# Kernel optimization log

Hardware: AMD Instinct MI355X
Metric: run time of the kernel (lower is better)

Reference implementation:

```python
import jax, jax.numpy as jnp
import numpy as np

N = 16384; C = 16; H = 256; W = 704
HEADS = 4; PTS = 4; K = 8; DH = C // HEADS
EPS = 1e-3  # BatchNorm eps from module

def _bn(x, g, b):
    # BatchNorm1d in training mode: batch statistics over N
    mu = x.mean(axis=0)
    var = x.var(axis=0)
    return (x - mu) * jax.lax.rsqrt(var + EPS) * g + b

def setup_inputs():
    key = jax.random.key(0)
    ks = jax.random.split(key, 20)
    def w(i, shape, s=0.25):
        return jax.random.normal(ks[i], shape, jnp.float32) * s
    grid_y = jax.random.randint(ks[0], (N,), 0, H)
    grid_x = jax.random.randint(ks[1], (N,), 0, W)
    return {
        "point_features": jax.random.normal(ks[2], (N, C), jnp.float32),
        "image_feat": jax.random.normal(ks[3], (C, H, W), jnp.float32),
        "image_grid": jnp.stack([grid_y, grid_x], axis=1),
        "Wk": w(4, (C, C)), "bk": w(5, (C,)), "gk": jnp.ones((C,)), "betak": jnp.zeros((C,)),
        "Wfc": w(6, (2, C)), "bfc": w(7, (C,)), "gfc": jnp.ones((C,)), "betafc": jnp.zeros((C,)),
        "Wt": w(8, (C, C)), "bt": w(9, (C,)), "gt": jnp.ones((C,)), "betat": jnp.zeros((C,)),
        "Woff": w(10, (C, HEADS * PTS * 2), 0.02), "boff": w(11, (HEADS * PTS * 2,), 0.5),
        "Wattn": w(12, (C, HEADS * PTS), 0.02), "battn": jnp.zeros((HEADS * PTS,)),
        "Wval": w(13, (C, C)), "bval": w(14, (C,)),
        "Wout": w(15, (C, C)), "bout": w(16, (C,)),
        "Wf": w(17, (2 * C, C)), "bf": w(18, (C,)), "gf": jnp.ones((C,)), "betaf": jnp.zeros((C,)),
    }

def _deform_attn(q, image_feat, grid_f, Woff, boff, Wattn, battn, Wval, bval, Wout, bout):
    # MSDeformAttn with 1 level: learned offsets around projected pixel, bilinear sampling
    n = q.shape[0]
    off = (q @ Woff + boff).reshape(n, HEADS, PTS, 2)
    attn = jax.nn.softmax((q @ Wattn + battn).reshape(n, HEADS, PTS), axis=-1)
    val = (image_feat.reshape(C, H * W).T @ Wval + bval).reshape(H * W, HEADS, DH)
    val_h = val.transpose(1, 0, 2)  # [HEADS, HW, DH]
    loc_y = grid_f[:, 0][:, None, None] + off[..., 0]  # [N, HEADS, PTS]
    loc_x = grid_f[:, 1][:, None, None] + off[..., 1]
    y0 = jnp.floor(loc_y); x0 = jnp.floor(loc_x)
    wy = loc_y - y0; wx = loc_x - x0

    def corner(yi, xi, wgt):
        valid = (yi >= 0) & (yi <= H - 1) & (xi >= 0) & (xi <= W - 1)
        yc = jnp.clip(yi, 0, H - 1).astype(jnp.int32)
        xc = jnp.clip(xi, 0, W - 1).astype(jnp.int32)
        idx = (yc * W + xc).transpose(1, 0, 2)  # [HEADS, N, PTS]
        g = jax.vmap(lambda v, i: v[i])(val_h, idx)  # [HEADS, N, PTS, DH]
        return g * (wgt * valid).transpose(1, 0, 2)[..., None]

    samp = (corner(y0, x0, (1 - wy) * (1 - wx))
            + corner(y0, x0 + 1, (1 - wy) * wx)
            + corner(y0 + 1, x0, wy * (1 - wx))
            + corner(y0 + 1, x0 + 1, wy * wx))  # [HEADS, N, PTS, DH]
    out = (samp * attn.transpose(1, 0, 2)[..., None]).sum(axis=2)  # [HEADS, N, DH]
    out = out.transpose(1, 0, 2).reshape(n, C)
    return out @ Wout + bout

def reference(point_features, image_feat, image_grid, Wk, bk, gk, betak, Wfc, bfc, gfc, betafc, Wt, bt, gt, betat, Woff, boff, Wattn, battn, Wval, bval, Wout, bout, Wf, bf, gf, betaf):
    grid_f = image_grid.astype(jnp.float32)
    # KNN over projected pixel coords (cKDTree.query k=K+1, drop self)
    d2 = ((grid_f[:, None, :] - grid_f[None, :, :]) ** 2).sum(-1)
    _, nidx = jax.lax.top_k(-d2, K + 1)
    nidx = nidx[:, 1:]  # [N, K]

    pts = _bn(point_features @ Wk + bk, gk, betak)  # pts_key_proj
    # normalized relative image-plane positions -> fc
    center = grid_f.mean(axis=0)
    rel = grid_f - center
    mx = jnp.abs(rel).max(axis=0)
    mx = jnp.where(mx == 0, 1.0, mx)
    pos = _bn((rel / mx) @ Wfc + bfc, gfc, betafc)

    # gather image feats at projected pixels + KNN-graph neighbor aggregation
    gathered = image_feat[:, image_grid[:, 0], image_grid[:, 1]].T  # [N, C]
    neigh = gathered[nidx].mean(axis=1)  # [N, C]

    q = pts + pos
    img_pre = _deform_attn(q, image_feat, grid_f, Woff, boff, Wattn, battn, Wval, bval, Wout, bout) + neigh

    pts_pre = _bn(pts @ Wt + bt, gt, betat)  # pts_transform
    fuse = jax.nn.relu(jnp.concatenate([pts_pre, img_pre], axis=-1))  # activate_out
    return jax.nn.relu(_bn(fuse @ Wf + bf, gf, betaf))  # fuse_conv
```

## Files before the change

kernel.cpp:

```cpp
#include <hip/hip_runtime.h>
#include <climits>

#define N_ 16384
#define C_ 16
#define H_ 256
#define W_ 704
#define HW_ (H_*W_)
#define NC_ (N_*C_)
#define EPS_ 1e-3f
#define HDR_ 512

typedef unsigned long long ull;


#define VAL_  (HDR_ + 9*NC_)
#define KNNI_ (VAL_ + HW_*16)
#define PARTF_ (KNNI_ + 378256)

__device__ __forceinline__ float wsum64(float v){
#pragma unroll
  for (int o = 32; o > 0; o >>= 1) v += __shfl_down(v, o);
  return v;
}

#define LOAD16(dst, src) { const float4* _s=(const float4*)(src); float4 _a=_s[0],_b=_s[1],_c=_s[2],_d=_s[3]; \
  dst[0]=_a.x;dst[1]=_a.y;dst[2]=_a.z;dst[3]=_a.w; dst[4]=_b.x;dst[5]=_b.y;dst[6]=_b.z;dst[7]=_b.w; \
  dst[8]=_c.x;dst[9]=_c.y;dst[10]=_c.z;dst[11]=_c.w; dst[12]=_d.x;dst[13]=_d.y;dst[14]=_d.z;dst[15]=_d.w; }

#define STORE16(dst, src) { float4* _d=(float4*)(dst); \
  _d[0]=make_float4(src[0],src[1],src[2],src[3]); _d[1]=make_float4(src[4],src[5],src[6],src[7]); \
  _d[2]=make_float4(src[8],src[9],src[10],src[11]); _d[3]=make_float4(src[12],src[13],src[14],src[15]); }

__global__ __launch_bounds__(256) void k_init(float* ws){
  if (blockIdx.x < 176){
    int4* c = (int4*)(ws + KNNI_);
    c[blockIdx.x*256 + threadIdx.x] = make_int4(0,0,0,0);
  } else if (threadIdx.x == 0){
    int* ih = (int*)ws;
    ih[0]=0; ih[1]=0; ih[2]=INT_MAX; ih[3]=INT_MIN; ih[4]=INT_MAX; ih[5]=INT_MIN;
  }
}

__global__ __launch_bounds__(256) void k_gridcnt(const int* __restrict__ grid, float* __restrict__ ws){
  int i = blockIdx.x*256 + threadIdx.x;
  int2 p = ((const int2*)grid)[i];
  int* counts = (int*)(ws + KNNI_);
  atomicAdd(&counts[p.x*W_ + p.y], 1);
  int sy=p.x, sx=p.y, mny=p.x, mxy=p.x, mnx=p.y, mxx=p.y;
#pragma unroll
  for (int o=32;o>0;o>>=1){
    sy += __shfl_down(sy,o); sx += __shfl_down(sx,o);
    mny = min(mny,__shfl_down(mny,o)); mxy = max(mxy,__shfl_down(mxy,o));
    mnx = min(mnx,__shfl_down(mnx,o)); mxx = max(mxx,__shfl_down(mxx,o));
  }
  __shared__ int sh[24];
  int w = threadIdx.x >> 6;
  if ((threadIdx.x & 63) == 0){
    sh[w]=sy; sh[4+w]=sx; sh[8+w]=mny; sh[12+w]=mxy; sh[16+w]=mnx; sh[20+w]=mxx;
  }
  __syncthreads();
  if (threadIdx.x == 0){
    int a0=sh[0]+sh[1]+sh[2]+sh[3];
    int a1=sh[4]+sh[5]+sh[6]+sh[7];
    int a2=min(min(sh[8],sh[9]),min(sh[10],sh[11]));
    int a3=max(max(sh[12],sh[13]),max(sh[14],sh[15]));
    int a4=min(min(sh[16],sh[17]),min(sh[18],sh[19]));
    int a5=max(max(sh[20],sh[21]),max(sh[22],sh[23]));
    int* ih = (int*)ws;
    atomicAdd(&ih[0],a0); atomicAdd(&ih[1],a1);
    atomicMin(&ih[2],a2); atomicMax(&ih[3],a3);
    atomicMin(&ih[4],a4); atomicMax(&ih[5],a5);
  }
}

__global__ __launch_bounds__(256) void k_scanA(float* ws){
  const int* counts = (const int*)(ws + KNNI_);
  int* bsum = (int*)(ws + KNNI_) + 180224 + 180240;
  int t = threadIdx.x;
  int v = counts[blockIdx.x*256 + t];
#pragma unroll
  for (int o=32;o>0;o>>=1) v += __shfl_down(v,o);
  __shared__ int w4[4];
  if ((t&63)==0) w4[t>>6] = v;
  __syncthreads();
  if (t==0) bsum[blockIdx.x] = w4[0]+w4[1]+w4[2]+w4[3];
}

__global__ __launch_bounds__(256) void k_scanB(float* ws){
  if (threadIdx.x == 0){
    int* ih = (int*)ws;
    float cy = (float)ih[0] / (float)N_;
    float cx = (float)ih[1] / (float)N_;
    float my = fmaxf((float)ih[3]-cy, cy-(float)ih[2]);
    float mx = fmaxf((float)ih[5]-cx, cx-(float)ih[4]);
    if (my == 0.f) my = 1.f;
    if (mx == 0.f) mx = 1.f;
    ws[264]=cy; ws[265]=cx; ws[266]=1.f/my; ws[267]=1.f/mx;
  }
  int* bsum = (int*)(ws + KNNI_) + 180224 + 180240;
  int* boff = bsum + 704;
  __shared__ int tmp[256];
  __shared__ int carry;
  int t = threadIdx.x;
  if (t==0) carry = 0;
  __syncthreads();
  for (int c=0;c<3;++c){
    int idx = c*256 + t;
    int v = (idx < 704) ? bsum[idx] : 0;
    tmp[t] = v;
    __syncthreads();
    for (int o=1;o<256;o<<=1){
      int x = (t>=o) ? tmp[t-o] : 0;
      __syncthreads();
      tmp[t] += x;
      __syncthreads();
    }
    int incl = tmp[t];
    int base = carry;
    if (idx < 704) boff[idx] = base + incl - v;
    __syncthreads();
    if (t==255) carry = base + incl;
    __syncthreads();
  }
}

__global__ __launch_bounds__(256) void k_scanC(float* ws){
  int* counts = (int*)(ws + KNNI_);
  int* cellst = counts + 180224;
  const int* boff = counts + 180224 + 180240 + 704;
  __shared__ int tmp[256];
  int t = threadIdx.x;
  int i = blockIdx.x*256 + t;
  int v = counts[i];
  tmp[t] = v;
  __syncthreads();
  for (int o=1;o<256;o<<=1){
    int x = (t>=o) ? tmp[t-o] : 0;
    __syncthreads();
    tmp[t] += x;
    __syncthreads();
  }
  int start = boff[blockIdx.x] + tmp[t] - v;
  cellst[i] = start;
  counts[i] = start;
  if (i == 0) cellst[HW_] = N_;
}

__global__ __launch_bounds__(256) void k_scatter(const int* __restrict__ grid, float* __restrict__ ws){
  int i = blockIdx.x*256 + threadIdx.x;
  int2 g = ((const int2*)grid)[i];
  int* counts = (int*)(ws + KNNI_);
  unsigned* psort = (unsigned*)(counts + 180224 + 180240 + 704 + 704);
  int pos = atomicAdd(&counts[g.x*W_ + g.y], 1);
  psort[pos] = ((unsigned)g.x<<24) | ((unsigned)g.y<<14) | (unsigned)i;
}

__global__ __launch_bounds__(256) void k_gath(const float* __restrict__ imf,
                                              const int* __restrict__ grid,
                                              float* __restrict__ ws){
  int idx = blockIdx.x*256 + threadIdx.x;
  int i = idx >> 4, c = idx & 15;
  int2 g = ((const int2*)grid)[i];
  ws[HDR_ + 2*NC_ + idx] = imf[c*HW_ + g.x*W_ + g.y];
}

__global__ __launch_bounds__(64) void k_knn2(float* __restrict__ ws){
  int gid = blockIdx.x*64 + threadIdx.x;
  const int* cellst = (const int*)(ws + KNNI_) + 180224;
  const unsigned* psort = (const unsigned*)((const int*)(ws + KNNI_) + 180224 + 180240 + 704 + 704);
  unsigned me = psort[gid];
  int y = (int)(me>>24), x = (int)((me>>14)&1023), i = (int)(me&16383);
  int r = 8;
  for (;;){
    int y0=max(y-r,0), y1=min(y+r,H_-1), x0=max(x-r,0), x1=min(x+r,W_-1);
    bool covered = (y0==0)&&(y1==H_-1)&&(x0==0)&&(x1==W_-1);
    int area = (y1-y0+1)*(x1-x0+1);
    if (area >= 224 || covered) break;
    r += 8;
  }
  ull arr[9];
  for (;;){
    int y0=max(y-r,0), y1=min(y+r,H_-1), x0=max(x-r,0), x1=min(x+r,W_-1);
    bool covered = (y0==0)&&(y1==H_-1)&&(x0==0)&&(x1==W_-1);
#pragma unroll
    for (int q=0;q<9;++q) arr[q] = ~0ull;
    for (int yy=y0; yy<=y1; ++yy){
      int rowb = yy*W_;
      int s = cellst[rowb + x0];
      int e = cellst[rowb + x1 + 1];
      for (int p=s; p<e; ++p){
        unsigned u = psort[p];
        int py = (int)(u>>24), px = (int)((u>>14)&1023), pi = (int)(u&16383);
        int dy = y-py, dx = x-px;
        int d2 = dy*dy + dx*dx;
        ull key = ((ull)(unsigned)d2 << 14) | (unsigned)pi;
        if (key < arr[8]){
          int q = 8;
          while (q > 0 && arr[q-1] > key){ arr[q] = arr[q-1]; --q; }
          arr[q] = key;
        }
      }
    }
    if (covered) break;
    if (arr[8] != ~0ull){
      int d9 = (int)(arr[8] >> 14);
      if (d9 < (r+1)*(r+1)) break;
    }
    r <<= 1;
  }
  const float* gath = ws + HDR_ + 2*NC_;
  float acc[16];
#pragma unroll
  for (int c=0;c<16;++c) acc[c] = 0.f;
  for (int nb=1; nb<9; ++nb){
    int idx = (int)(arr[nb] & 16383ull);
    const float4* s4 = (const float4*)(gath + idx*16);
#pragma unroll
    for (int rq=0; rq<4; ++rq){
      float4 v = s4[rq];
      acc[rq*4]+=v.x; acc[rq*4+1]+=v.y; acc[rq*4+2]+=v.z; acc[rq*4+3]+=v.w;
    }
  }
  float* neigh = ws + HDR_ + 7*NC_;
  float o[16];
#pragma unroll
  for (int c=0;c<16;++c) o[c] = acc[c]*0.125f;
  STORE16(neigh + i*16, o);
}

__global__ __launch_bounds__(64) void k_lin1(
    const float* __restrict__ pf, const int* __restrict__ grid,
    const float* __restrict__ Wk, const float* __restrict__ bk,
    const float* __restrict__ Wfc, const float* __restrict__ bfc,
    float* __restrict__ ws)
{
  __shared__ float sWk[256], sbk[16], sWfc[32], sbfc[16];
  int t = threadIdx.x;
  for (int j=t;j<256;j+=64) sWk[j] = Wk[j];
  if (t < 16){ sbk[t]=bk[t]; sbfc[t]=bfc[t]; }
  if (t < 32) sWfc[t] = Wfc[t];
  __syncthreads();
  int i = blockIdx.x*64 + t;
  float p[16]; LOAD16(p, pf + i*16);
  float ok[16];
#pragma unroll
  for (int c=0;c<16;++c) ok[c] = sbk[c];
#pragma unroll
  for (int j=0;j<16;++j){ float v = p[j];
#pragma unroll
    for (int c=0;c<16;++c) ok[c] += v*sWk[j*16+c];
  }
  float* pts_lin = ws + HDR_;
  STORE16(pts_lin + i*16, ok);
  float cy=ws[264], cx=ws[265], imy=ws[266], imx=ws[267];
  int2 g = ((const int2*)grid)[i];
  float ry = ((float)g.x - cy)*imy, rx = ((float)g.y - cx)*imx;
  float op[16];
#pragma unroll
  for (int c=0;c<16;++c) op[c] = ry*sWfc[c] + rx*sWfc[16+c] + sbfc[c];
  float* pos_lin = ws + HDR_ + NC_;
  STORE16(pos_lin + i*16, op);
  float* partK  = ws + VAL_;
  float* partFC = ws + VAL_ + 8192;
#pragma unroll
  for (int c=0;c<16;++c){
    float a = wsum64(ok[c]); float b = wsum64(ok[c]*ok[c]);
    if (t==0){ partK[blockIdx.x*32+c]=a; partK[blockIdx.x*32+16+c]=b; }
    a = wsum64(op[c]); b = wsum64(op[c]*op[c]);
    if (t==0){ partFC[blockIdx.x*32+c]=a; partFC[blockIdx.x*32+16+c]=b; }
  }
}

__device__ __forceinline__ void red1_body(const float* __restrict__ g, const float* __restrict__ b,
                                          float* __restrict__ ws, int partOff, int aOff, float* red){
  int t = threadIdx.x, slot = t & 31, chunk = t >> 5;
  const float* part = ws + partOff;
  float acc = 0.f;
  for (int bb=chunk*32; bb<chunk*32+32; ++bb) acc += part[bb*32 + slot];
  red[t] = acc;
  __syncthreads();
  if (chunk == 0){
    float v = red[slot];
#pragma unroll
    for (int k2=1;k2<8;++k2) v += red[k2*32+slot];
    red[slot] = v;
  }
  __syncthreads();
  if (t < 16){
    float mu  = red[t]    * (1.f/N_);
    float var = red[16+t] * (1.f/N_) - mu*mu;
    float a = g[t] / sqrtf(var + EPS_);
    ws[aOff+t]    = a;
    ws[aOff+16+t] = b[t] - mu*a;
  }
  __syncthreads();
}

__global__ __launch_bounds__(256) void k_red2(const float* __restrict__ gk, const float* __restrict__ betak,
                                              const float* __restrict__ gfc, const float* __restrict__ betafc,
                                              float* __restrict__ ws){
  __shared__ float red[256];
  red1_body(gk, betak, ws, VAL_, 136, red);
  red1_body(gfc, betafc, ws, VAL_+8192, 168, red);
}

__global__ __launch_bounds__(256) void k_red1(const float* __restrict__ g, const float* __restrict__ b,
                                              float* __restrict__ ws, int partOff, int aOff){
  __shared__ float red[256];
  red1_body(g, b, ws, partOff, aOff, red);
}

__global__ __launch_bounds__(64) void k_qstage(
    const float* __restrict__ Wt, const float* __restrict__ bt,
    const float* __restrict__ Woff, const float* __restrict__ boff,
    const float* __restrict__ Wattn, const float* __restrict__ battn,
    float* __restrict__ ws)
{
  __shared__ float sWt[256], sWoff[512], sWattn[256];
  __shared__ float sbt[16], sboff[32], sbattn[16];
  __shared__ float skA[16], skC[16], sfcA[16], sfcC[16];
  int t = threadIdx.x;
  for (int j=t;j<256;j+=64){ sWt[j]=Wt[j]; sWattn[j]=Wattn[j]; }
  for (int j=t;j<512;j+=64) sWoff[j]=Woff[j];
  if (t<16){ sbt[t]=bt[t]; sbattn[t]=battn[t];
    skA[t]=ws[136+t]; skC[t]=ws[152+t]; sfcA[t]=ws[168+t]; sfcC[t]=ws[184+t]; }
  if (t<32) sboff[t]=boff[t];
  __syncthreads();
  int i = blockIdx.x*64 + t;
  float* pts_lin = ws + HDR_;
  float* pos_lin = ws + HDR_ + NC_;
  float* t_lin   = ws + HDR_ + 3*NC_;
  float* offp    = ws + HDR_ + 4*NC_;
  float* attnp   = ws + HDR_ + 6*NC_;
  float pl[16], po[16];
  LOAD16(pl, pts_lin + i*16);
  LOAD16(po, pos_lin + i*16);
  float pts[16], q[16];
#pragma unroll
  for (int c=0;c<16;++c){ pts[c] = pl[c]*skA[c]+skC[c]; q[c] = pts[c] + po[c]*sfcA[c]+sfcC[c]; }
  float tv[16];
#pragma unroll
  for (int c=0;c<16;++c) tv[c] = sbt[c];
#pragma unroll
  for (int j=0;j<16;++j){ float v=pts[j];
#pragma unroll
    for (int c=0;c<16;++c) tv[c] += v*sWt[j*16+c];
  }
  STORE16(t_lin + i*16, tv);
  float* partT = ws + VAL_ + 16384;
#pragma unroll
  for (int c=0;c<16;++c){
    float a = wsum64(tv[c]); float b = wsum64(tv[c]*tv[c]);
    if (t==0){ partT[blockIdx.x*32+c]=a; partT[blockIdx.x*32+16+c]=b; }
  }
  float ov[32];
#pragma unroll
  for (int o=0;o<32;++o) ov[o] = sboff[o];
#pragma unroll
  for (int j=0;j<16;++j){ float v=q[j];
#pragma unroll
    for (int o=0;o<32;++o) ov[o] += v*sWoff[j*32+o];
  }
  { float4* d=(float4*)(offp + i*32);
#pragma unroll
    for (int r=0;r<8;++r) d[r]=make_float4(ov[r*4],ov[r*4+1],ov[r*4+2],ov[r*4+3]);
  }
  float l[16];
#pragma unroll
  for (int c=0;c<16;++c) l[c] = sbattn[c];
#pragma unroll
  for (int j=0;j<16;++j){ float v=q[j];
#pragma unroll
    for (int c=0;c<16;++c) l[c] += v*sWattn[j*16+c];
  }
  float av[16];
#pragma unroll
  for (int h=0;h<4;++h){
    float m = fmaxf(fmaxf(l[h*4],l[h*4+1]),fmaxf(l[h*4+2],l[h*4+3]));
    float e0=expf(l[h*4]-m), e1=expf(l[h*4+1]-m), e2=expf(l[h*4+2]-m), e3=expf(l[h*4+3]-m);
    float inv = 1.f/(e0+e1+e2+e3);
    av[h*4]=e0*inv; av[h*4+1]=e1*inv; av[h*4+2]=e2*inv; av[h*4+3]=e3*inv;
  }
  STORE16(attnp + i*16, av);
}

__global__ __launch_bounds__(256) void k_val(const float* __restrict__ imf,
    const float* __restrict__ Wval, const float* __restrict__ bval, float* __restrict__ ws)
{
  __shared__ float sW[256], sb[16];
  int t = threadIdx.x;
  sW[t] = Wval[t];
  if (t < 16) sb[t] = bval[t];
  __syncthreads();
  int pix = blockIdx.x*256 + t;
  float a[16];
#pragma unroll
  for (int ci=0;ci<16;++ci) a[ci] = imf[ci*HW_ + pix];
  float o[16];
#pragma unroll
  for (int c=0;c<16;++c) o[c] = sb[c];
#pragma unroll
  for (int ci=0;ci<16;++ci){ float v=a[ci];
#pragma unroll
    for (int c=0;c<16;++c) o[c] += v*sW[ci*16+c];
  }
  float* val = ws + VAL_;
  STORE16(val + pix*16, o);
}

__global__ __launch_bounds__(256) void k_attn(
    const int* __restrict__ grid,
    const float* __restrict__ Wout, const float* __restrict__ bout,
    const float* __restrict__ Wf, const float* __restrict__ bf,
    float* __restrict__ ws)
{
  __shared__ float sWout[256], sWf[512], sbout[16], sbf[16];
  __shared__ float sTl[1024], sNei[1024], sSamp[1024], sImg[1024];
  __shared__ float sPart[128];
  int t = threadIdx.x;
  int p = t >> 2, h = t & 3;
  int i = blockIdx.x*64 + p;
  sWout[t]=Wout[t]; sWf[t]=Wf[t]; sWf[t+256]=Wf[t+256];
  if (t<16){ sbout[t]=bout[t]; sbf[t]=bf[t]; }
  {
    const float4* tl4 = (const float4*)(ws + HDR_ + 3*NC_ + blockIdx.x*1024);
    const float4* nv4 = (const float4*)(ws + HDR_ + 7*NC_ + blockIdx.x*1024);
    float4 v = tl4[t];
    int c0 = (t*4) & 15;
    float a0=ws[200+c0],a1=ws[200+c0+1],a2=ws[200+c0+2],a3=ws[200+c0+3];
    float c0v=ws[216+c0],c1v=ws[216+c0+1],c2v=ws[216+c0+2],c3v=ws[216+c0+3];
    sTl[t*4]   = fmaxf(v.x*a0+c0v, 0.f);
    sTl[t*4+1] = fmaxf(v.y*a1+c1v, 0.f);
    sTl[t*4+2] = fmaxf(v.z*a2+c2v, 0.f);
    sTl[t*4+3] = fmaxf(v.w*a3+c3v, 0.f);
    float4 nv = nv4[t];
    sNei[t*4]=nv.x; sNei[t*4+1]=nv.y; sNei[t*4+2]=nv.z; sNei[t*4+3]=nv.w;
  }
  const float4* off4 = (const float4*)(ws + HDR_ + 4*NC_ + blockIdx.x*2048);
  float4 o0 = off4[t*2], o1 = off4[t*2+1];
  float4 aw = ((const float4*)(ws + HDR_ + 6*NC_ + blockIdx.x*1024))[t];
  int2 g = ((const int2*)grid)[i];
  float y = (float)g.x, x = (float)g.y;
  const float4* val4 = (const float4*)(ws + VAL_);
  float4 acc = make_float4(0.f,0.f,0.f,0.f);
  float offv[8] = {o0.x,o0.y,o0.z,o0.w,o1.x,o1.y,o1.z,o1.w};
  float avv[4]  = {aw.x,aw.y,aw.z,aw.w};
#define CORNER(yy,xx,wgt) do{ int _y=(yy),_x=(xx); \
    if ((unsigned)_y < (unsigned)H_ && (unsigned)_x < (unsigned)W_){ \
      float4 _v = val4[(_y*W_+_x)*4 + h]; float _w = a*(wgt); \
      acc.x += _w*_v.x; acc.y += _w*_v.y; acc.z += _w*_v.z; acc.w += _w*_v.w; } }while(0)
#pragma unroll
  for (int pt=0; pt<4; ++pt){
    float a  = avv[pt];
    float ly = y + offv[pt*2], lx = x + offv[pt*2+1];
    float fy = floorf(ly), fx = floorf(lx);
    float wy = ly - fy, wx = lx - fx;
    int y0 = (int)fy, x0 = (int)fx;
    CORNER(y0,   x0,   (1.f-wy)*(1.f-wx));
    CORNER(y0,   x0+1, (1.f-wy)*wx);
    CORNER(y0+1, x0,   wy*(1.f-wx));
    CORNER(y0+1, x0+1, wy*wx);
  }
#undef CORNER
  ((float4*)sSamp)[t] = acc;
  __syncthreads();
  float img[4];
#pragma unroll
  for (int k=0;k<4;++k){ int cc=h*4+k; img[k] = sbout[cc] + sNei[p*16+cc]; }
#pragma unroll
  for (int j=0;j<16;++j){
    float v = sSamp[p*16+j];
#pragma unroll
    for (int k=0;k<4;++k) img[k] += v*sWout[j*16 + h*4 + k];
  }
  ((float4*)sImg)[t] = make_float4(img[0],img[1],img[2],img[3]);
  __syncthreads();
  float fl[4];
#pragma unroll
  for (int k=0;k<4;++k) fl[k] = sbf[h*4+k];
#pragma unroll
  for (int j=0;j<16;++j){
    float v1 = sTl[p*16+j];
    float v2 = fmaxf(sImg[p*16+j], 0.f);
#pragma unroll
    for (int k=0;k<4;++k){
      fl[k] += v1*sWf[j*16 + h*4 + k];
      fl[k] += v2*sWf[(16+j)*16 + h*4 + k];
    }
  }
  float* f_lin = ws + HDR_ + 8*NC_;
  ((float4*)(f_lin + blockIdx.x*1024))[t] = make_float4(fl[0],fl[1],fl[2],fl[3]);
  float s0=fl[0],s1=fl[1],s2=fl[2],s3=fl[3];
  float q0=fl[0]*fl[0],q1=fl[1]*fl[1],q2=fl[2]*fl[2],q3=fl[3]*fl[3];
#pragma unroll
  for (int o=32;o>=4;o>>=1){
    s0+=__shfl_down(s0,o); s1+=__shfl_down(s1,o); s2+=__shfl_down(s2,o); s3+=__shfl_down(s3,o);
    q0+=__shfl_down(q0,o); q1+=__shfl_down(q1,o); q2+=__shfl_down(q2,o); q3+=__shfl_down(q3,o);
  }
  int wave = t >> 6, lane = t & 63;
  if (lane < 4){
    sPart[wave*32 + lane*4+0]=s0; sPart[wave*32 + lane*4+1]=s1;
    sPart[wave*32 + lane*4+2]=s2; sPart[wave*32 + lane*4+3]=s3;
    sPart[wave*32 + 16 + lane*4+0]=q0; sPart[wave*32 + 16 + lane*4+1]=q1;
    sPart[wave*32 + 16 + lane*4+2]=q2; sPart[wave*32 + 16 + lane*4+3]=q3;
  }
  __syncthreads();
  if (t < 32){
    float v = sPart[t]+sPart[32+t]+sPart[64+t]+sPart[96+t];
    (ws + PARTF_)[blockIdx.x*32 + t] = v;
  }
}

__global__ __launch_bounds__(256) void k_out(const float* __restrict__ ws, float* __restrict__ out){
  int idx = blockIdx.x*256 + threadIdx.x;
  int c = idx & 15;
  float v = ws[HDR_ + 8*NC_ + idx];
  out[idx] = fmaxf(v*ws[232+c] + ws[248+c], 0.f);
}

extern "C" void kernel_launch(void* const* d_in, const int* in_sizes, int n_in,
                              void* d_out, int out_size, void* d_ws, size_t ws_size,
                              hipStream_t stream)
{
  const float* pf    = (const float*)d_in[0];
  const float* imf   = (const float*)d_in[1];
  const int*   gridp = (const int*)d_in[2];
  const float* Wk   =(const float*)d_in[3],  *bk   =(const float*)d_in[4];
  const float* gk   =(const float*)d_in[5],  *betak=(const float*)d_in[6];
  const float* Wfc  =(const float*)d_in[7],  *bfc  =(const float*)d_in[8];
  const float* gfc  =(const float*)d_in[9],  *betafc=(const float*)d_in[10];
  const float* Wt   =(const float*)d_in[11], *bt   =(const float*)d_in[12];
  const float* gt   =(const float*)d_in[13], *betat=(const float*)d_in[14];
  const float* Woff =(const float*)d_in[15], *boff =(const float*)d_in[16];
  const float* Wattn=(const float*)d_in[17], *battn=(const float*)d_in[18];
  const float* Wval =(const float*)d_in[19], *bval =(const float*)d_in[20];
  const float* Wout =(const float*)d_in[21], *bout =(const float*)d_in[22];
  const float* Wf   =(const float*)d_in[23], *bf   =(const float*)d_in[24];
  const float* gf   =(const float*)d_in[25], *betaf=(const float*)d_in[26];
  float* ws  = (float*)d_ws;
  float* out = (float*)d_out;

  hipLaunchKernelGGL(k_init,     dim3(177),     dim3(256), 0, stream, ws);
  hipLaunchKernelGGL(k_gridcnt,  dim3(N_/256),  dim3(256), 0, stream, gridp, ws);
  hipLaunchKernelGGL(k_scanA,    dim3(704),     dim3(256), 0, stream, ws);
  hipLaunchKernelGGL(k_scanB,    dim3(1),       dim3(256), 0, stream, ws);
  hipLaunchKernelGGL(k_scanC,    dim3(704),     dim3(256), 0, stream, ws);
  hipLaunchKernelGGL(k_scatter,  dim3(N_/256),  dim3(256), 0, stream, gridp, ws);
  hipLaunchKernelGGL(k_gath,     dim3(NC_/256), dim3(256), 0, stream, imf, gridp, ws);
  hipLaunchKernelGGL(k_lin1,     dim3(N_/64),   dim3(64),  0, stream, pf, gridp, Wk, bk, Wfc, bfc, ws);
  hipLaunchKernelGGL(k_red2,     dim3(1),       dim3(256), 0, stream, gk, betak, gfc, betafc, ws);
  hipLaunchKernelGGL(k_qstage,   dim3(N_/64),   dim3(64),  0, stream, Wt, bt, Woff, boff, Wattn, battn, ws);
  hipLaunchKernelGGL(k_red1,     dim3(1),       dim3(256), 0, stream, gt, betat, ws, VAL_+16384, 200);
  hipLaunchKernelGGL(k_val,      dim3(HW_/256), dim3(256), 0, stream, imf, Wval, bval, ws);
  hipLaunchKernelGGL(k_knn2,     dim3(N_/64),   dim3(64),  0, stream, ws);
  hipLaunchKernelGGL(k_attn,     dim3(N_/64),   dim3(256), 0, stream, gridp, Wout, bout, Wf, bf, ws);
  hipLaunchKernelGGL(k_red1,     dim3(1),       dim3(256), 0, stream, gf, betaf, ws, PARTF_, 232);
  hipLaunchKernelGGL(k_out,      dim3(NC_/256), dim3(256), 0, stream, ws, out);
}
```

Before: 275.0 us.

## Split each KNN query across four threads with shared-memory top-k merge

The KNN kernel now uses four lanes per query point, each scanning every fourth row of the search window and keeping a partial top-9 list. The lists are merged through shared memory by lane 0, which also decides whether to double the radius, and block-wide barriers coordinate the iterations. The final neighbour-feature averaging is split so each lane handles four channels. The aim is more parallelism and shorter per-thread serial scans, at the cost of extra barriers, shared-memory traffic, and whole blocks iterating until their slowest query finishes.

```diff
diff --git a/kernel.cpp b/kernel.cpp
--- a/kernel.cpp
+++ b/kernel.cpp
@@ -164,8 +164,15 @@
   ws[HDR_ + 2*NC_ + idx] = imf[c*HW_ + g.x*W_ + g.y];
 }
 
-__global__ __launch_bounds__(64) void k_knn2(float* __restrict__ ws){
-  int gid = blockIdx.x*64 + threadIdx.x;
+__global__ __launch_bounds__(256) void k_knn3(float* __restrict__ ws){
+  __shared__ ull sK[256*9];
+  __shared__ int sNb[64*8];
+  __shared__ int sR[64];
+  __shared__ int sDoneP[64];
+  __shared__ int sUndone;
+  int tid = threadIdx.x;
+  int s = tid & 3, pl = tid >> 2;
+  int gid = blockIdx.x*64 + pl;
   const int* cellst = (const int*)(ws + KNNI_) + 180224;
   const unsigned* psort = (const unsigned*)((const int*)(ws + KNNI_) + 180224 + 180240 + 704 + 704);
   unsigned me = psort[gid];
@@ -178,54 +185,79 @@
     if (area >= 224 || covered) break;
     r += 8;
   }
-  ull arr[9];
+  if (s == 0){ sR[pl] = r; sDoneP[pl] = 0; }
+  if (tid == 0) sUndone = 0;
+  __syncthreads();
   for (;;){
+    r = sR[pl];
+    bool active = (sDoneP[pl] == 0);
     int y0=max(y-r,0), y1=min(y+r,H_-1), x0=max(x-r,0), x1=min(x+r,W_-1);
-    bool covered = (y0==0)&&(y1==H_-1)&&(x0==0)&&(x1==W_-1);
+    ull arr[9];
 #pragma unroll
     for (int q=0;q<9;++q) arr[q] = ~0ull;
-    for (int yy=y0; yy<=y1; ++yy){
-      int rowb = yy*W_;
-      int s = cellst[rowb + x0];
-      int e = cellst[rowb + x1 + 1];
-      for (int p=s; p<e; ++p){
-        unsigned u = psort[p];
-        int py = (int)(u>>24), px = (int)((u>>14)&1023), pi = (int)(u&16383);
-        int dy = y-py, dx = x-px;
-        int d2 = dy*dy + dx*dx;
-        ull key = ((ull)(unsigned)d2 << 14) | (unsigned)pi;
-        if (key < arr[8]){
-          int q = 8;
-          while (q > 0 && arr[q-1] > key){ arr[q] = arr[q-1]; --q; }
-          arr[q] = key;
+    if (active){
+      for (int yy=y0+s; yy<=y1; yy+=4){
+        int rowb = yy*W_;
+        int st = cellst[rowb + x0];
+        int e  = cellst[rowb + x1 + 1];
+        for (int p=st; p<e; ++p){
+          unsigned u = psort[p];
+          int py = (int)(u>>24), px = (int)((u>>14)&1023), pi = (int)(u&16383);
+          int dy = y-py, dx = x-px;
+          int d2 = dy*dy + dx*dx;
+          ull key = ((ull)(unsigned)d2 << 14) | (unsigned)pi;
+          if (key < arr[8]){
+            int q = 8;
+            while (q > 0 && arr[q-1] > key){ arr[q] = arr[q-1]; --q; }
+            arr[q] = key;
+          }
         }
       }
+#pragma unroll
+      for (int q=0;q<9;++q) sK[tid*9+q] = arr[q];
     }
-    if (covered) break;
-    if (arr[8] != ~0ull){
-      int d9 = (int)(arr[8] >> 14);
-      if (d9 < (r+1)*(r+1)) break;
+    __syncthreads();
+    if (active && s == 0){
+      for (int ss=1; ss<4; ++ss){
+        for (int q2=0; q2<9; ++q2){
+          ull k = sK[(tid+ss)*9+q2];
+          if (k >= arr[8]) break;
+          int q = 8;
+          while (q > 0 && arr[q-1] > k){ arr[q] = arr[q-1]; --q; }
+          arr[q] = k;
+        }
+      }
+      bool covered = (y0==0)&&(y1==H_-1)&&(x0==0)&&(x1==W_-1);
+      bool ok = covered;
+      if (!ok && arr[8] != ~0ull){
+        int d9 = (int)(arr[8] >> 14);
+        ok = d9 < (r+1)*(r+1);
+      }
+      if (ok){
+        sDoneP[pl] = 1;
+#pragma unroll
+        for (int q=1;q<9;++q) sNb[pl*8 + q-1] = (int)(arr[q] & 16383ull);
+      } else {
+        sR[pl] = r << 1;
+        atomicAdd(&sUndone, 1);
+      }
     }
-    r <<= 1;
+    __syncthreads();
+    int undone = sUndone;
+    __syncthreads();
+    if (undone == 0) break;
+    if (tid == 0) sUndone = 0;
   }
   const float* gath = ws + HDR_ + 2*NC_;
-  float acc[16];
-#pragma unroll
-  for (int c=0;c<16;++c) acc[c] = 0.f;
-  for (int nb=1; nb<9; ++nb){
-    int idx = (int)(arr[nb] & 16383ull);
-    const float4* s4 = (const float4*)(gath + idx*16);
-#pragma unroll
-    for (int rq=0; rq<4; ++rq){
-      float4 v = s4[rq];
-      acc[rq*4]+=v.x; acc[rq*4+1]+=v.y; acc[rq*4+2]+=v.z; acc[rq*4+3]+=v.w;
-    }
+  float4 acc = make_float4(0.f,0.f,0.f,0.f);
+#pragma unroll
+  for (int nb=0; nb<8; ++nb){
+    const float4 g = *(const float4*)(gath + sNb[pl*8+nb]*16 + s*4);
+    acc.x += g.x; acc.y += g.y; acc.z += g.z; acc.w += g.w;
   }
   float* neigh = ws + HDR_ + 7*NC_;
-  float o[16];
-#pragma unroll
-  for (int c=0;c<16;++c) o[c] = acc[c]*0.125f;
-  STORE16(neigh + i*16, o);
+  *(float4*)(neigh + i*16 + s*4) =
+      make_float4(acc.x*0.125f, acc.y*0.125f, acc.z*0.125f, acc.w*0.125f);
 }
 
 __global__ __launch_bounds__(64) void k_lin1(
@@ -552,7 +584,7 @@
   hipLaunchKernelGGL(k_qstage,   dim3(N_/64),   dim3(64),  0, stream, Wt, bt, Woff, boff, Wattn, battn, ws);
   hipLaunchKernelGGL(k_red1,     dim3(1),       dim3(256), 0, stream, gt, betat, ws, VAL_+16384, 200);
   hipLaunchKernelGGL(k_val,      dim3(HW_/256), dim3(256), 0, stream, imf, Wval, bval, ws);
-  hipLaunchKernelGGL(k_knn2,     dim3(N_/64),   dim3(64),  0, stream, ws);
+  hipLaunchKernelGGL(k_knn3,     dim3(N_/64),   dim3(256), 0, stream, ws);
   hipLaunchKernelGGL(k_attn,     dim3(N_/64),   dim3(256), 0, stream, gridp, Wout, bout, Wf, bf, ws);
   hipLaunchKernelGGL(k_red1,     dim3(1),       dim3(256), 0, stream, gf, betaf, ws, PARTF_, 232);
   hipLaunchKernelGGL(k_out,      dim3(NC_/256), dim3(256), 0, stream, ws, out);
```

Result: faster. 225.7 us (-17.9%).
